# Optimization experiments

Measured on AMD Instinct MI355X. Metric: run time of the kernel, lower is better.

The kernel has to match this reference:

```python
import jax, jax.numpy as jnp
import numpy as np

N_NODES = 100000
NEG_SLOPE = 0.01  # F.leaky_relu default


def _hetero_graphconv(x, src, dst, W, b, n_nodes):
    """HeteroGraphConv(aggregate='sum') of DGL GraphConv(norm='both') per edge type.

    x: [N, d_in]; src/dst: [R, E] int; W: [R, d_in, d_out]; b: [R, d_out].
    """
    n_rel = W.shape[0]
    ones = None
    out = jnp.zeros((n_nodes, W.shape[2]), dtype=x.dtype)
    for r in range(n_rel):  # small fixed number of relations
        s, d = src[r], dst[r]
        e_ones = jnp.ones(s.shape, dtype=x.dtype)
        deg_out = jnp.clip(jax.ops.segment_sum(e_ones, s, num_segments=n_nodes), 1.0)
        deg_in = jnp.clip(jax.ops.segment_sum(e_ones, d, num_segments=n_nodes), 1.0)
        # norm='both': scale src by out_deg^-1/2, aggregate, scale dst by in_deg^-1/2.
        # Apply weight before gather (aggregation is linear) to shrink edge traffic.
        h = (x * (deg_out ** -0.5)[:, None]) @ W[r]          # [N, d_out]
        agg = jax.ops.segment_sum(h[s], d, num_segments=n_nodes)  # gather-scatter over edges
        out = out + agg * (deg_in ** -0.5)[:, None] + b[r]
    return out


def setup_inputs() -> dict:
    key = jax.random.key(0)
    ks = jax.random.split(key, 8)
    d_in, d_h, d_out, n_cls, n_rel, n_edges = 256, 128, 128, 16, 3, 600000
    x = jax.random.normal(ks[0], (N_NODES, d_in), dtype=jnp.float32)
    src = jax.random.randint(ks[1], (n_rel, n_edges), 0, N_NODES, dtype=jnp.int32)
    dst = jax.random.randint(ks[2], (n_rel, n_edges), 0, N_NODES, dtype=jnp.int32)
    W0 = jax.random.normal(ks[3], (n_rel, d_in, d_h), dtype=jnp.float32) * (d_in ** -0.5)
    b0 = jnp.zeros((n_rel, d_h), dtype=jnp.float32)
    W1 = jax.random.normal(ks[4], (n_rel, d_h, d_out), dtype=jnp.float32) * (d_h ** -0.5)
    b1 = jnp.zeros((n_rel, d_out), dtype=jnp.float32)
    fc_W = jax.random.normal(ks[5], (d_out, n_cls), dtype=jnp.float32) * (d_out ** -0.5)
    fc_b = jnp.zeros((n_cls,), dtype=jnp.float32)
    return {"x": x, "src": src, "dst": dst, "W0": W0, "b0": b0,
            "W1": W1, "b1": b1, "fc_W": fc_W, "fc_b": fc_b}


def reference(x, src, dst, W0, b0, W1, b1, fc_W, fc_b):
    n = x.shape[0]
    h = _hetero_graphconv(x, src, dst, W0, b0, n)
    h = jax.nn.leaky_relu(h, negative_slope=NEG_SLOPE)  # dropout rate 0 (eval)
    h = _hetero_graphconv(h, src, dst, W1, b1, n)       # last layer: no activation
    logits = h @ fc_W + fc_b
    return (h, logits)
```

## Files before the change

kernel.cpp:

```cpp
#include <hip/hip_runtime.h>
#include <hip/hip_bf16.h>
#include <stdint.h>


typedef __attribute__((ext_vector_type(8))) short bf16x8;
typedef __attribute__((ext_vector_type(4))) float f32x4;
typedef unsigned short u16;

#define SCAN_T 256
#define SCAN_E 8
#define SCAN_BLK (SCAN_T * SCAN_E)
#define CUR_PAD 16
#define BF_K 8
#define HIST_K 4
#define NSLOT 12

__global__ __launch_bounds__(256)
void hist_kernel(const int* __restrict__ src, const int* __restrict__ dst,
                 int* __restrict__ cnt_out8, int* __restrict__ cnt_in8,
                 int E, int N) {
    int r = blockIdx.y;
    int e0 = blockIdx.x * (256 * HIST_K) + threadIdx.x;
    int copy = blockIdx.x & 7;
    size_t base = ((size_t)copy * 3 + r) * N;
    int s[HIST_K], d[HIST_K];
#pragma unroll
    for (int j = 0; j < HIST_K; j++) {
        int e = e0 + j * 256;
        bool v = e < E;
        s[j] = v ? src[(size_t)r * E + e] : -1;
        d[j] = v ? dst[(size_t)r * E + e] : -1;
    }
#pragma unroll
    for (int j = 0; j < HIST_K; j++)
        if (s[j] >= 0) atomicAdd(cnt_out8 + base + s[j], 1);
#pragma unroll
    for (int j = 0; j < HIST_K; j++)
        if (d[j] >= 0) atomicAdd(cnt_in8 + base + d[j], 1);
}

__global__ __launch_bounds__(256)
void reduce_scales_kernel(const int* __restrict__ cnt_out8, const int* __restrict__ cnt_in8,
                          float* __restrict__ s_out, float* __restrict__ s_in,
                          int* __restrict__ cnt_all, int N) {
    int n = blockIdx.x * blockDim.x + threadIdx.x;
    if (n >= N) return;
    int tot = 0;
#pragma unroll
    for (int r = 0; r < 3; r++) {
        int co = 0, ci = 0;
#pragma unroll
        for (int c = 0; c < 8; c++) {
            co += cnt_out8[((size_t)c * 3 + r) * N + n];
            ci += cnt_in8[((size_t)c * 3 + r) * N + n];
        }
        s_out[(size_t)r * N + n] = rsqrtf(fmaxf((float)co, 1.0f));
        s_in[(size_t)r * N + n]  = rsqrtf(fmaxf((float)ci, 1.0f));
        tot += ci;
    }
    cnt_all[n] = tot;
}

__global__ __launch_bounds__(SCAN_T)
void scan1_kernel(const int* __restrict__ cnt, int* __restrict__ pre,
                  int* __restrict__ bsums, int N) {
    int b = blockIdx.x, t = threadIdx.x;
    int base = b * SCAN_BLK + t * SCAN_E;
    int v[SCAN_E], s = 0;
#pragma unroll
    for (int j = 0; j < SCAN_E; j++) {
        int idx = base + j;
        v[j] = (idx < N) ? cnt[idx] : 0;
        s += v[j];
    }
    __shared__ int sd[SCAN_T];
    sd[t] = s;
    __syncthreads();
    for (int off = 1; off < SCAN_T; off <<= 1) {
        int x = (t >= off) ? sd[t - off] : 0;
        __syncthreads();
        sd[t] += x;
        __syncthreads();
    }
    if (t == SCAN_T - 1) bsums[b] = sd[t];
    int run = sd[t] - s;
#pragma unroll
    for (int j = 0; j < SCAN_E; j++) {
        int idx = base + j;
        if (idx < N) pre[idx] = run;
        run += v[j];
    }
}

__global__ void scan2_kernel(int* __restrict__ bsums, int* __restrict__ row_start,
                             int nb, int N) {
    int run = 0;
    for (int b = 0; b < nb; b++) {
        int t = bsums[b];
        bsums[b] = run;
        run += t;
    }
    row_start[N] = run;
}

__global__ __launch_bounds__(SCAN_T)
void scan3_kernel(int* __restrict__ pre, const int* __restrict__ bsums,
                  int* __restrict__ cursor, int nb, int N) {
    int b = blockIdx.x, t = threadIdx.x;
    int add = bsums[b];
    int base = b * SCAN_BLK + t * SCAN_E;
#pragma unroll
    for (int j = 0; j < SCAN_E; j++) {
        int idx = base + j;
        if (idx < N) {
            int val = pre[idx] + add;
            pre[idx] = val;
            cursor[(size_t)idx * CUR_PAD] = val;
        }
    }
}

__global__ __launch_bounds__(256)
void bucket_fill_kernel(const int* __restrict__ src, const int* __restrict__ dst,
                        int* __restrict__ cursor, int* __restrict__ esrc,
                        int E, int N) {
    int r = blockIdx.y;
    int e0 = blockIdx.x * (256 * BF_K) + threadIdx.x;
    int s[BF_K], d[BF_K], pos[BF_K];
#pragma unroll
    for (int j = 0; j < BF_K; j++) {
        int e = e0 + j * 256;
        bool v = e < E;
        s[j] = v ? src[(size_t)r * E + e] : -1;
        d[j] = v ? dst[(size_t)r * E + e] : 0;
    }
#pragma unroll
    for (int j = 0; j < BF_K; j++)
        pos[j] = (s[j] >= 0) ? atomicAdd(cursor + (size_t)d[j] * CUR_PAD, 1) : 0;
#pragma unroll
    for (int j = 0; j < BF_K; j++)
        if (s[j] >= 0) esrc[pos[j]] = r * N + s[j];
}

__global__ __launch_bounds__(256)
void prep_w_kernel(const float* __restrict__ W0, const float* __restrict__ W1,
                   u16* __restrict__ w0hi, u16* __restrict__ w0lo,
                   u16* __restrict__ w1hi, u16* __restrict__ w1lo) {
    int idx = blockIdx.x * blockDim.x + threadIdx.x;
    const int n0 = 3 * 256 * 128;
    const int n1 = 3 * 128 * 128;
    if (idx >= n0 + n1) return;
    float f;
    u16 *phi, *plo;
    int oidx;
    if (idx < n0) {
        int r = idx / 32768, rem = idx % 32768;
        int n = rem / 256, k = rem % 256;
        f = W0[(size_t)r * 32768 + (size_t)k * 128 + n];
        phi = w0hi; plo = w0lo; oidx = idx;
    } else {
        int i2 = idx - n0;
        int r = i2 / 16384, rem = i2 % 16384;
        int n = rem / 128, k = rem % 128;
        f = W1[(size_t)r * 16384 + (size_t)k * 128 + n];
        phi = w1hi; plo = w1lo; oidx = i2;
    }
    uint32_t u = __float_as_uint(f);
    phi[oidx] = (u16)(u >> 16);
    float lo = f - __uint_as_float(u & 0xFFFF0000u);
    uint32_t ul = __float_as_uint(lo);
    plo[oidx] = (u16)((ul + 0x7FFFu + ((ul >> 16) & 1u)) >> 16);
}

__global__ __launch_bounds__(256)
void gemm_split_bf16(const float* __restrict__ A, const float* __restrict__ s_out,
                     const u16* __restrict__ Whi_all, const u16* __restrict__ Wlo_all,
                     u16* __restrict__ Cout_all, int M, int K, int Nn) {
    const int r = blockIdx.y;
    const float* scale = s_out + (size_t)r * Nn;
    const u16* Whi = Whi_all + (size_t)r * K * 128;
    const u16* Wlo = Wlo_all + (size_t)r * K * 128;
    u16* Cout = Cout_all + (size_t)r * Nn * 128;

    __shared__ u16 As_hi[128][40];
    __shared__ u16 As_lo[128][40];
    __shared__ u16 Bs_hi[128][40];
    __shared__ u16 Bs_lo[128][40];

    const int tid  = threadIdx.x;
    const int m0   = blockIdx.x * 128;
    const int lane = tid & 63;
    const int wave = tid >> 6;
    const int wm   = (wave & 1) * 64;
    const int wn   = (wave >> 1) * 64;
    const int lm   = lane & 15;
    const int kq   = (lane >> 4) * 8;

    f32x4 acc[4][4];
#pragma unroll
    for (int i = 0; i < 4; i++)
#pragma unroll
        for (int j = 0; j < 4; j++) acc[i][j] = (f32x4){0.f, 0.f, 0.f, 0.f};

    const int srow = tid >> 1;
    const int skb  = (tid & 1) * 16;

    const bool valid = (m0 + srow) < M;
    const float sval = valid ? scale[m0 + srow] : 0.f;
    const float* arow = A + (size_t)(m0 + srow) * K;
    const u16* whrow = Whi + (size_t)srow * K;
    const u16* wlrow = Wlo + (size_t)srow * K;

    for (int k0 = 0; k0 < K; k0 += 32) {
        float fa[16];
        if (valid) {
            *(float4*)&fa[0]  = *(const float4*)(arow + k0 + skb);
            *(float4*)&fa[4]  = *(const float4*)(arow + k0 + skb + 4);
            *(float4*)&fa[8]  = *(const float4*)(arow + k0 + skb + 8);
            *(float4*)&fa[12] = *(const float4*)(arow + k0 + skb + 12);
        } else {
#pragma unroll
            for (int i = 0; i < 16; i++) fa[i] = 0.f;
        }
        uint32_t ah[8], al[8];
#pragma unroll
        for (int p = 0; p < 8; p++) {
            float f0 = fa[2 * p] * sval, f1 = fa[2 * p + 1] * sval;
            uint32_t u0 = __float_as_uint(f0), u1 = __float_as_uint(f1);
            ah[p] = (u0 >> 16) | (u1 & 0xFFFF0000u);
            float l0 = f0 - __uint_as_float(u0 & 0xFFFF0000u);
            float l1 = f1 - __uint_as_float(u1 & 0xFFFF0000u);
            al[p] = (__float_as_uint(l0) >> 16) | (__float_as_uint(l1) & 0xFFFF0000u);
        }
        *(uint4*)&As_hi[srow][skb]     = *(uint4*)&ah[0];
        *(uint4*)&As_hi[srow][skb + 8] = *(uint4*)&ah[4];
        *(uint4*)&As_lo[srow][skb]     = *(uint4*)&al[0];
        *(uint4*)&As_lo[srow][skb + 8] = *(uint4*)&al[4];

        *(uint4*)&Bs_hi[srow][skb]     = *(const uint4*)(whrow + k0 + skb);
        *(uint4*)&Bs_hi[srow][skb + 8] = *(const uint4*)(whrow + k0 + skb + 8);
        *(uint4*)&Bs_lo[srow][skb]     = *(const uint4*)(wlrow + k0 + skb);
        *(uint4*)&Bs_lo[srow][skb + 8] = *(const uint4*)(wlrow + k0 + skb + 8);

        __syncthreads();

        bf16x8 a_hi[4], a_lo[4], b_hi[4], b_lo[4];
#pragma unroll
        for (int i = 0; i < 4; i++) {
            a_hi[i] = *(const bf16x8*)&As_hi[wm + i * 16 + lm][kq];
            a_lo[i] = *(const bf16x8*)&As_lo[wm + i * 16 + lm][kq];
            b_hi[i] = *(const bf16x8*)&Bs_hi[wn + i * 16 + lm][kq];
            b_lo[i] = *(const bf16x8*)&Bs_lo[wn + i * 16 + lm][kq];
        }
#pragma unroll
        for (int i = 0; i < 4; i++)
#pragma unroll
            for (int j = 0; j < 4; j++) {
                acc[i][j] = __builtin_amdgcn_mfma_f32_16x16x32_bf16(a_hi[i], b_hi[j], acc[i][j], 0, 0, 0);
                acc[i][j] = __builtin_amdgcn_mfma_f32_16x16x32_bf16(a_lo[i], b_hi[j], acc[i][j], 0, 0, 0);
                acc[i][j] = __builtin_amdgcn_mfma_f32_16x16x32_bf16(a_hi[i], b_lo[j], acc[i][j], 0, 0, 0);
            }
        __syncthreads();
    }

    const int rq = (lane >> 4) * 4;
#pragma unroll
    for (int i = 0; i < 4; i++) {
        int mbase = m0 + wm + i * 16 + rq;
#pragma unroll
        for (int j = 0; j < 4; j++) {
            int col = wn + j * 16 + lm;
#pragma unroll
            for (int rg = 0; rg < 4; rg++) {
                int m = mbase + rg;
                if (m < M) {
                    uint32_t u = __float_as_uint(acc[i][j][rg]);
                    Cout[(size_t)m * 128 + col] =
                        (u16)((u + 0x7FFFu + ((u >> 16) & 1u)) >> 16);
                }
            }
        }
    }
}

#define BF16_LO(u) __uint_as_float((u) << 16)
#define BF16_HI(u) __uint_as_float((u) & 0xFFFF0000u)

__device__ __forceinline__ void gather_pair(const uint32_t* __restrict__ hb32,
                                            const int* __restrict__ row_start,
                                            const int* __restrict__ esrc,
                                            const float* __restrict__ s_in,
                                            int snodeA, int nodeBr, int half,
                                            int lane31, int N, float acc[4]) {
    const int N2 = N * 2;
    const int snodeB = (nodeBr < N) ? nodeBr : (N - 1);
    const int begA = __builtin_amdgcn_readfirstlane(row_start[snodeA]);
    const int endA = __builtin_amdgcn_readfirstlane(row_start[snodeA + 1]);
    const int begB = __builtin_amdgcn_readfirstlane(row_start[snodeB]);
    const int endB = __builtin_amdgcn_readfirstlane(row_start[snodeB + 1]);
    const int degA = endA - begA, degB = endB - begB;
    const int maxdeg = degA > degB ? degA : degB;

    float wA0 = s_in[snodeA], wA1 = s_in[(size_t)N + snodeA], wA2 = s_in[(size_t)N2 + snodeA];
    float wB0 = s_in[snodeB], wB1 = s_in[(size_t)N + snodeB], wB2 = s_in[(size_t)N2 + snodeB];
    if (nodeBr >= N) { wB0 = 0.f; wB1 = 0.f; wB2 = 0.f; }

    const float w0 = half ? wB0 : wA0;
    const float w1 = half ? wB1 : wA1;
    const float w2 = half ? wB2 : wA2;
    const int   deg = half ? degB : degA;
    const uint32_t* hcol = hb32 + lane31 * 2;

    for (int j = 0; j < maxdeg; j += NSLOT) {
        uint2 u[NSLOT];
        float w[NSLOT];
#pragma unroll
        for (int p = 0; p < NSLOT; p++) {
            int iA = esrc[begA + j + p];
            int iB = esrc[begB + j + p];
            int idx = half ? iB : iA;
            float ws = (idx < N) ? w0 : ((idx < N2) ? w1 : w2);
            bool act = (j + p) < deg;
            w[p] = act ? ws : 0.f;
            idx = act ? idx : 0;
            u[p] = *(const uint2*)(hcol + (size_t)idx * 64);
        }
#pragma unroll
        for (int p = 0; p < NSLOT; p++) {
            acc[0] = fmaf(BF16_LO(u[p].x), w[p], acc[0]);
            acc[1] = fmaf(BF16_HI(u[p].x), w[p], acc[1]);
            acc[2] = fmaf(BF16_LO(u[p].y), w[p], acc[2]);
            acc[3] = fmaf(BF16_HI(u[p].y), w[p], acc[3]);
        }
    }
}

__global__ __launch_bounds__(256)
void gather_l0(const u16* __restrict__ hb, const int* __restrict__ row_start,
               const int* __restrict__ esrc, const float* __restrict__ s_in,
               const float* __restrict__ b, float* __restrict__ out, int N) {
    int wv = threadIdx.x >> 6;
    int t = threadIdx.x & 63;
    int half = t >> 5;
    int lane31 = t & 31;
    int snodeA = __builtin_amdgcn_readfirstlane(blockIdx.x * 8 + wv * 2);
    if (snodeA >= N) return;
    int nodeBr = snodeA + 1;
    float acc[4] = {0.f, 0.f, 0.f, 0.f};
    gather_pair((const uint32_t*)hb, row_start, esrc, s_in,
                snodeA, nodeBr, half, lane31, N, acc);
    int node = half ? nodeBr : snodeA;
    int c0 = lane31 * 4;
    float4 b0v = *(const float4*)(b + c0);
    float4 b1v = *(const float4*)(b + 128 + c0);
    float4 b2v = *(const float4*)(b + 256 + c0);
    float bs[4] = {b0v.x + b1v.x + b2v.x, b0v.y + b1v.y + b2v.y,
                   b0v.z + b1v.z + b2v.z, b0v.w + b1v.w + b2v.w};
    float4 o;
    float* po = (float*)&o;
#pragma unroll
    for (int k = 0; k < 4; k++) {
        float v = acc[k] + bs[k];
        po[k] = fmaxf(v, 0.f) + 0.01f * fminf(v, 0.f);
    }
    if (node < N) *(float4*)(out + (size_t)node * 128 + c0) = o;
}

__global__ __launch_bounds__(256)
void gather_l1(const u16* __restrict__ hb, const int* __restrict__ row_start,
               const int* __restrict__ esrc, const float* __restrict__ s_in,
               const float* __restrict__ b, const float* __restrict__ fcW,
               const float* __restrict__ fcb, float* __restrict__ out_h,
               float* __restrict__ out_logits, int N) {
    int wv = threadIdx.x >> 6;
    int t = threadIdx.x & 63;
    int half = t >> 5;
    int lane31 = t & 31;
    int snodeA = __builtin_amdgcn_readfirstlane(blockIdx.x * 8 + wv * 2);
    if (snodeA >= N) return;
    int nodeBr = snodeA + 1;
    float acc[4] = {0.f, 0.f, 0.f, 0.f};
    gather_pair((const uint32_t*)hb, row_start, esrc, s_in,
                snodeA, nodeBr, half, lane31, N, acc);
    int node = half ? nodeBr : snodeA;
    int c0 = lane31 * 4;
    float4 b0v = *(const float4*)(b + c0);
    float4 b1v = *(const float4*)(b + 128 + c0);
    float4 b2v = *(const float4*)(b + 256 + c0);
    float v[4] = {acc[0] + b0v.x + b1v.x + b2v.x, acc[1] + b0v.y + b1v.y + b2v.y,
                  acc[2] + b0v.z + b1v.z + b2v.z, acc[3] + b0v.w + b1v.w + b2v.w};
    if (node < N) {
        float4 o = make_float4(v[0], v[1], v[2], v[3]);
        *(float4*)(out_h + (size_t)node * 128 + c0) = o;
    }

    float p[16];
#pragma unroll
    for (int jj = 0; jj < 16; jj++) {
        p[jj] = v[0] * fcW[(size_t)(c0 + 0) * 16 + jj]
              + v[1] * fcW[(size_t)(c0 + 1) * 16 + jj]
              + v[2] * fcW[(size_t)(c0 + 2) * 16 + jj]
              + v[3] * fcW[(size_t)(c0 + 3) * 16 + jj];
    }
#pragma unroll
    for (int off = 1; off <= 16; off <<= 1) {
#pragma unroll
        for (int jj = 0; jj < 16; jj++) p[jj] += __shfl_xor(p[jj], off);
    }
    if (lane31 == 0 && node < N) {
        float* lp = out_logits + (size_t)node * 16;
        *(float4*)(lp + 0)  = make_float4(p[0] + fcb[0],  p[1] + fcb[1],  p[2] + fcb[2],  p[3] + fcb[3]);
        *(float4*)(lp + 4)  = make_float4(p[4] + fcb[4],  p[5] + fcb[5],  p[6] + fcb[6],  p[7] + fcb[7]);
        *(float4*)(lp + 8)  = make_float4(p[8] + fcb[8],  p[9] + fcb[9],  p[10] + fcb[10], p[11] + fcb[11]);
        *(float4*)(lp + 12) = make_float4(p[12] + fcb[12], p[13] + fcb[13], p[14] + fcb[14], p[15] + fcb[15]);
    }
}

extern "C" void kernel_launch(void* const* d_in, const int* in_sizes, int n_in,
                              void* d_out, int out_size, void* d_ws, size_t ws_size,
                              hipStream_t stream) {
    const float* x   = (const float*)d_in[0];
    const int*   src = (const int*)d_in[1];
    const int*   dst = (const int*)d_in[2];
    const float* W0  = (const float*)d_in[3];
    const float* b0  = (const float*)d_in[4];
    const float* W1  = (const float*)d_in[5];
    const float* b1  = (const float*)d_in[6];
    const float* fcW = (const float*)d_in[7];
    const float* fcb = (const float*)d_in[8];

    const int N = in_sizes[0] / 256;
    const int E = in_sizes[1] / 3;
    const int nb = (N + SCAN_BLK - 1) / SCAN_BLK;

    float* out_h      = (float*)d_out;
    float* out_logits = out_h + (size_t)N * 128;

    char* p = (char*)d_ws;
    auto alloc = [&](size_t bytes) -> char* {
        char* q = p;
        p += (bytes + 255) & ~(size_t)255;
        return q;
    };
    float* s_out     = (float*)alloc(3 * (size_t)N * 4);
    float* s_in      = (float*)alloc(3 * (size_t)N * 4);
    int*   cnt8      = (int*)alloc(2 * 8 * 3 * (size_t)N * 4);
    int*   cnt_out8  = cnt8;
    int*   cnt_in8   = cnt8 + 8 * 3 * (size_t)N;
    int*   cnt_all   = (int*)alloc((size_t)N * 4);
    int*   row_start = (int*)alloc((size_t)(N + 1) * 4);
    int*   cursor    = (int*)alloc((size_t)N * CUR_PAD * 4);
    int*   bsums     = (int*)alloc(1024 * 4);
    int*   esrc      = (int*)alloc(3 * (size_t)E * 4 + 1024);
    u16*   w0hi      = (u16*)alloc(3 * 256 * 128 * 2);
    u16*   w0lo      = (u16*)alloc(3 * 256 * 128 * 2);
    u16*   w1hi      = (u16*)alloc(3 * 128 * 128 * 2);
    u16*   w1lo      = (u16*)alloc(3 * 128 * 128 * 2);
    u16*   hb        = (u16*)alloc(3 * (size_t)N * 128 * 2);
    float* acc0      = (float*)alloc((size_t)N * 128 * 4);

    hipMemsetAsync(cnt8, 0, 2 * 8 * 3 * (size_t)N * sizeof(int), stream);

    hist_kernel<<<dim3((E + 256 * HIST_K - 1) / (256 * HIST_K), 3), 256, 0, stream>>>(
        src, dst, cnt_out8, cnt_in8, E, N);
    reduce_scales_kernel<<<(N + 255) / 256, 256, 0, stream>>>(
        cnt_out8, cnt_in8, s_out, s_in, cnt_all, N);

    scan1_kernel<<<nb, SCAN_T, 0, stream>>>(cnt_all, row_start, bsums, N);
    scan2_kernel<<<1, 1, 0, stream>>>(bsums, row_start, nb, N);
    scan3_kernel<<<nb, SCAN_T, 0, stream>>>(row_start, bsums, cursor, nb, N);
    bucket_fill_kernel<<<dim3((E + 256 * BF_K - 1) / (256 * BF_K), 3), 256, 0, stream>>>(
        src, dst, cursor, esrc, E, N);

    prep_w_kernel<<<(3 * 256 * 128 + 3 * 128 * 128 + 255) / 256, 256, 0, stream>>>(
        W0, W1, w0hi, w0lo, w1hi, w1lo);

    int gemm_blocks   = (N + 127) / 128;
    int gather_blocks = (N + 7) / 8;

    gemm_split_bf16<<<dim3(gemm_blocks, 3), 256, 0, stream>>>(
        x, s_out, w0hi, w0lo, hb, N, 256, N);
    gather_l0<<<gather_blocks, 256, 0, stream>>>(hb, row_start, esrc, s_in, b0, acc0, N);

    gemm_split_bf16<<<dim3(gemm_blocks, 3), 256, 0, stream>>>(
        acc0, s_out, w1hi, w1lo, hb, N, 128, N);
    gather_l1<<<gather_blocks, 256, 0, stream>>>(hb, row_start, esrc, s_in, b1, fcW, fcb,
                                                 out_h, out_logits, N);
}
```

Before: 768.1 us.

## Merge per-relation GEMMs into one block sharing A tile; move out-degree scale to gather

The three per-relation GEMM launches are merged into one 768-thread block. The A tile (x or acc0) is loaded and split into hi/lo bf16 once and shared by three wave groups, each using its own relation's weights, which cuts A reads and conversion work by three. Because the A tile is now shared, the per-relation out-degree scale can no longer be applied to it, so it moves into the gather as a per-edge multiply by s_out[src]. This adds an extra scattered load per edge. Output stores in the last layer become nontemporal.

```diff
diff --git a/kernel.cpp b/kernel.cpp
--- a/kernel.cpp
+++ b/kernel.cpp
@@ -172,27 +172,23 @@
     plo[oidx] = (u16)((ul + 0x7FFFu + ((ul >> 16) & 1u)) >> 16);
 }
 
-__global__ __launch_bounds__(256)
-void gemm_split_bf16(const float* __restrict__ A, const float* __restrict__ s_out,
-                     const u16* __restrict__ Whi_all, const u16* __restrict__ Wlo_all,
-                     u16* __restrict__ Cout_all, int M, int K, int Nn) {
-    const int r = blockIdx.y;
-    const float* scale = s_out + (size_t)r * Nn;
-    const u16* Whi = Whi_all + (size_t)r * K * 128;
-    const u16* Wlo = Wlo_all + (size_t)r * K * 128;
-    u16* Cout = Cout_all + (size_t)r * Nn * 128;
-
+__global__ __launch_bounds__(768)
+void gemm_merged(const float* __restrict__ A,
+                 const u16* __restrict__ Whi_all, const u16* __restrict__ Wlo_all,
+                 u16* __restrict__ Cout_all, int M, int K, int Nn) {
     __shared__ u16 As_hi[128][40];
     __shared__ u16 As_lo[128][40];
-    __shared__ u16 Bs_hi[128][40];
-    __shared__ u16 Bs_lo[128][40];
+    __shared__ u16 Bs_hi[3][128][40];
+    __shared__ u16 Bs_lo[3][128][40];
 
     const int tid  = threadIdx.x;
     const int m0   = blockIdx.x * 128;
     const int lane = tid & 63;
     const int wave = tid >> 6;
-    const int wm   = (wave & 1) * 64;
-    const int wn   = (wave >> 1) * 64;
+    const int wr   = wave >> 2;
+    const int wq   = wave & 3;
+    const int wm   = (wq & 1) * 64;
+    const int wn   = (wq >> 1) * 64;
     const int lm   = lane & 15;
     const int kq   = (lane >> 4) * 8;
 
@@ -202,46 +198,57 @@
 #pragma unroll
         for (int j = 0; j < 4; j++) acc[i][j] = (f32x4){0.f, 0.f, 0.f, 0.f};
 
-    const int srow = tid >> 1;
-    const int skb  = (tid & 1) * 16;
-
-    const bool valid = (m0 + srow) < M;
-    const float sval = valid ? scale[m0 + srow] : 0.f;
-    const float* arow = A + (size_t)(m0 + srow) * K;
-    const u16* whrow = Whi + (size_t)srow * K;
-    const u16* wlrow = Wlo + (size_t)srow * K;
+    const int srowA = tid >> 1;
+    const int skbA  = (tid & 1) * 16;
+    const bool validA = (tid < 256) && ((m0 + srowA) < M);
+    const float* arow = A + (size_t)(m0 + srowA) * K;
+
+    const int bslot = tid - 256;
 
     for (int k0 = 0; k0 < K; k0 += 32) {
-        float fa[16];
-        if (valid) {
-            *(float4*)&fa[0]  = *(const float4*)(arow + k0 + skb);
-            *(float4*)&fa[4]  = *(const float4*)(arow + k0 + skb + 4);
-            *(float4*)&fa[8]  = *(const float4*)(arow + k0 + skb + 8);
-            *(float4*)&fa[12] = *(const float4*)(arow + k0 + skb + 12);
+        if (tid < 256) {
+            float fa[16];
+            if (validA) {
+                *(float4*)&fa[0]  = *(const float4*)(arow + k0 + skbA);
+                *(float4*)&fa[4]  = *(const float4*)(arow + k0 + skbA + 4);
+                *(float4*)&fa[8]  = *(const float4*)(arow + k0 + skbA + 8);
+                *(float4*)&fa[12] = *(const float4*)(arow + k0 + skbA + 12);
+            } else {
+#pragma unroll
+                for (int i = 0; i < 16; i++) fa[i] = 0.f;
+            }
+            uint32_t ah[8], al[8];
+#pragma unroll
+            for (int p = 0; p < 8; p++) {
+                float f0 = fa[2 * p], f1 = fa[2 * p + 1];
+                uint32_t u0 = __float_as_uint(f0), u1 = __float_as_uint(f1);
+                ah[p] = (u0 >> 16) | (u1 & 0xFFFF0000u);
+                float l0 = f0 - __uint_as_float(u0 & 0xFFFF0000u);
+                float l1 = f1 - __uint_as_float(u1 & 0xFFFF0000u);
+                al[p] = (__float_as_uint(l0) >> 16) | (__float_as_uint(l1) & 0xFFFF0000u);
+            }
+            *(uint4*)&As_hi[srowA][skbA]     = *(uint4*)&ah[0];
+            *(uint4*)&As_hi[srowA][skbA + 8] = *(uint4*)&ah[4];
+            *(uint4*)&As_lo[srowA][skbA]     = *(uint4*)&al[0];
+            *(uint4*)&As_lo[srowA][skbA + 8] = *(uint4*)&al[4];
         } else {
 #pragma unroll
-            for (int i = 0; i < 16; i++) fa[i] = 0.f;
-        }
-        uint32_t ah[8], al[8];
-#pragma unroll
-        for (int p = 0; p < 8; p++) {
-            float f0 = fa[2 * p] * sval, f1 = fa[2 * p + 1] * sval;
-            uint32_t u0 = __float_as_uint(f0), u1 = __float_as_uint(f1);
-            ah[p] = (u0 >> 16) | (u1 & 0xFFFF0000u);
-            float l0 = f0 - __uint_as_float(u0 & 0xFFFF0000u);
-            float l1 = f1 - __uint_as_float(u1 & 0xFFFF0000u);
-            al[p] = (__float_as_uint(l0) >> 16) | (__float_as_uint(l1) & 0xFFFF0000u);
-        }
-        *(uint4*)&As_hi[srow][skb]     = *(uint4*)&ah[0];
-        *(uint4*)&As_hi[srow][skb + 8] = *(uint4*)&ah[4];
-        *(uint4*)&As_lo[srow][skb]     = *(uint4*)&al[0];
-        *(uint4*)&As_lo[srow][skb + 8] = *(uint4*)&al[4];
-
-        *(uint4*)&Bs_hi[srow][skb]     = *(const uint4*)(whrow + k0 + skb);
-        *(uint4*)&Bs_hi[srow][skb + 8] = *(const uint4*)(whrow + k0 + skb + 8);
-        *(uint4*)&Bs_lo[srow][skb]     = *(const uint4*)(wlrow + k0 + skb);
-        *(uint4*)&Bs_lo[srow][skb + 8] = *(const uint4*)(wlrow + k0 + skb + 8);
-
+            for (int c = 0; c < 2; c++) {
+                int slot = bslot + c * 512;
+                if (slot < 768) {
+                    int r    = slot >> 8;
+                    int s2   = slot & 255;
+                    int srow = s2 >> 1;
+                    int skb  = (s2 & 1) * 16;
+                    const u16* wh = Whi_all + ((size_t)r * 128 + srow) * K;
+                    const u16* wl = Wlo_all + ((size_t)r * 128 + srow) * K;
+                    *(uint4*)&Bs_hi[r][srow][skb]     = *(const uint4*)(wh + k0 + skb);
+                    *(uint4*)&Bs_hi[r][srow][skb + 8] = *(const uint4*)(wh + k0 + skb + 8);
+                    *(uint4*)&Bs_lo[r][srow][skb]     = *(const uint4*)(wl + k0 + skb);
+                    *(uint4*)&Bs_lo[r][srow][skb + 8] = *(const uint4*)(wl + k0 + skb + 8);
+                }
+            }
+        }
         __syncthreads();
 
         bf16x8 a_hi[4], a_lo[4], b_hi[4], b_lo[4];
@@ -249,8 +256,8 @@
         for (int i = 0; i < 4; i++) {
             a_hi[i] = *(const bf16x8*)&As_hi[wm + i * 16 + lm][kq];
             a_lo[i] = *(const bf16x8*)&As_lo[wm + i * 16 + lm][kq];
-            b_hi[i] = *(const bf16x8*)&Bs_hi[wn + i * 16 + lm][kq];
-            b_lo[i] = *(const bf16x8*)&Bs_lo[wn + i * 16 + lm][kq];
+            b_hi[i] = *(const bf16x8*)&Bs_hi[wr][wn + i * 16 + lm][kq];
+            b_lo[i] = *(const bf16x8*)&Bs_lo[wr][wn + i * 16 + lm][kq];
         }
 #pragma unroll
         for (int i = 0; i < 4; i++)
@@ -263,6 +270,7 @@
         __syncthreads();
     }
 
+    u16* Cout = Cout_all + (size_t)wr * Nn * 128;
     const int rq = (lane >> 4) * 4;
 #pragma unroll
     for (int i = 0; i < 4; i++) {
@@ -290,6 +298,7 @@
                                             const int* __restrict__ row_start,
                                             const int* __restrict__ esrc,
                                             const float* __restrict__ s_in,
+                                            const float* __restrict__ s_out,
                                             int snodeA, int nodeBr, int half,
                                             int lane31, int N, float acc[4]) {
     const int N2 = N * 2;
@@ -321,8 +330,9 @@
             int idx = half ? iB : iA;
             float ws = (idx < N) ? w0 : ((idx < N2) ? w1 : w2);
             bool act = (j + p) < deg;
-            w[p] = act ? ws : 0.f;
             idx = act ? idx : 0;
+            float so = s_out[idx];
+            w[p] = act ? ws * so : 0.f;
             u[p] = *(const uint2*)(hcol + (size_t)idx * 64);
         }
 #pragma unroll
@@ -338,6 +348,7 @@
 __global__ __launch_bounds__(256)
 void gather_l0(const u16* __restrict__ hb, const int* __restrict__ row_start,
                const int* __restrict__ esrc, const float* __restrict__ s_in,
+               const float* __restrict__ s_out,
                const float* __restrict__ b, float* __restrict__ out, int N) {
     int wv = threadIdx.x >> 6;
     int t = threadIdx.x & 63;
@@ -347,7 +358,7 @@
     if (snodeA >= N) return;
     int nodeBr = snodeA + 1;
     float acc[4] = {0.f, 0.f, 0.f, 0.f};
-    gather_pair((const uint32_t*)hb, row_start, esrc, s_in,
+    gather_pair((const uint32_t*)hb, row_start, esrc, s_in, s_out,
                 snodeA, nodeBr, half, lane31, N, acc);
     int node = half ? nodeBr : snodeA;
     int c0 = lane31 * 4;
@@ -356,19 +367,19 @@
     float4 b2v = *(const float4*)(b + 256 + c0);
     float bs[4] = {b0v.x + b1v.x + b2v.x, b0v.y + b1v.y + b2v.y,
                    b0v.z + b1v.z + b2v.z, b0v.w + b1v.w + b2v.w};
-    float4 o;
-    float* po = (float*)&o;
+    f32x4 o;
 #pragma unroll
     for (int k = 0; k < 4; k++) {
         float v = acc[k] + bs[k];
-        po[k] = fmaxf(v, 0.f) + 0.01f * fminf(v, 0.f);
-    }
-    if (node < N) *(float4*)(out + (size_t)node * 128 + c0) = o;
+        o[k] = fmaxf(v, 0.f) + 0.01f * fminf(v, 0.f);
+    }
+    if (node < N) *(f32x4*)(out + (size_t)node * 128 + c0) = o;
 }
 
 __global__ __launch_bounds__(256)
 void gather_l1(const u16* __restrict__ hb, const int* __restrict__ row_start,
                const int* __restrict__ esrc, const float* __restrict__ s_in,
+               const float* __restrict__ s_out,
                const float* __restrict__ b, const float* __restrict__ fcW,
                const float* __restrict__ fcb, float* __restrict__ out_h,
                float* __restrict__ out_logits, int N) {
@@ -380,7 +391,7 @@
     if (snodeA >= N) return;
     int nodeBr = snodeA + 1;
     float acc[4] = {0.f, 0.f, 0.f, 0.f};
-    gather_pair((const uint32_t*)hb, row_start, esrc, s_in,
+    gather_pair((const uint32_t*)hb, row_start, esrc, s_in, s_out,
                 snodeA, nodeBr, half, lane31, N, acc);
     int node = half ? nodeBr : snodeA;
     int c0 = lane31 * 4;
@@ -390,8 +401,8 @@
     float v[4] = {acc[0] + b0v.x + b1v.x + b2v.x, acc[1] + b0v.y + b1v.y + b2v.y,
                   acc[2] + b0v.z + b1v.z + b2v.z, acc[3] + b0v.w + b1v.w + b2v.w};
     if (node < N) {
-        float4 o = make_float4(v[0], v[1], v[2], v[3]);
-        *(float4*)(out_h + (size_t)node * 128 + c0) = o;
+        f32x4 o = {v[0], v[1], v[2], v[3]};
+        __builtin_nontemporal_store(o, (f32x4*)(out_h + (size_t)node * 128 + c0));
     }
 
     float p[16];
@@ -409,10 +420,14 @@
     }
     if (lane31 == 0 && node < N) {
         float* lp = out_logits + (size_t)node * 16;
-        *(float4*)(lp + 0)  = make_float4(p[0] + fcb[0],  p[1] + fcb[1],  p[2] + fcb[2],  p[3] + fcb[3]);
-        *(float4*)(lp + 4)  = make_float4(p[4] + fcb[4],  p[5] + fcb[5],  p[6] + fcb[6],  p[7] + fcb[7]);
-        *(float4*)(lp + 8)  = make_float4(p[8] + fcb[8],  p[9] + fcb[9],  p[10] + fcb[10], p[11] + fcb[11]);
-        *(float4*)(lp + 12) = make_float4(p[12] + fcb[12], p[13] + fcb[13], p[14] + fcb[14], p[15] + fcb[15]);
+        f32x4 q0 = {p[0] + fcb[0],  p[1] + fcb[1],  p[2] + fcb[2],  p[3] + fcb[3]};
+        f32x4 q1 = {p[4] + fcb[4],  p[5] + fcb[5],  p[6] + fcb[6],  p[7] + fcb[7]};
+        f32x4 q2 = {p[8] + fcb[8],  p[9] + fcb[9],  p[10] + fcb[10], p[11] + fcb[11]};
+        f32x4 q3 = {p[12] + fcb[12], p[13] + fcb[13], p[14] + fcb[14], p[15] + fcb[15]};
+        __builtin_nontemporal_store(q0, (f32x4*)(lp + 0));
+        __builtin_nontemporal_store(q1, (f32x4*)(lp + 4));
+        __builtin_nontemporal_store(q2, (f32x4*)(lp + 8));
+        __builtin_nontemporal_store(q3, (f32x4*)(lp + 12));
     }
 }
 
@@ -478,12 +493,11 @@
     int gemm_blocks   = (N + 127) / 128;
     int gather_blocks = (N + 7) / 8;
 
-    gemm_split_bf16<<<dim3(gemm_blocks, 3), 256, 0, stream>>>(
-        x, s_out, w0hi, w0lo, hb, N, 256, N);
-    gather_l0<<<gather_blocks, 256, 0, stream>>>(hb, row_start, esrc, s_in, b0, acc0, N);
-
-    gemm_split_bf16<<<dim3(gemm_blocks, 3), 256, 0, stream>>>(
-        acc0, s_out, w1hi, w1lo, hb, N, 128, N);
-    gather_l1<<<gather_blocks, 256, 0, stream>>>(hb, row_start, esrc, s_in, b1, fcW, fcb,
-                                                 out_h, out_logits, N);
-}
+    gemm_merged<<<gemm_blocks, 768, 0, stream>>>(x, w0hi, w0lo, hb, N, 256, N);
+    gather_l0<<<gather_blocks, 256, 0, stream>>>(hb, row_start, esrc, s_in, s_out,
+                                                 b0, acc0, N);
+
+    gemm_merged<<<gemm_blocks, 768, 0, stream>>>(acc0, w1hi, w1lo, hb, N, 128, N);
+    gather_l1<<<gather_blocks, 256, 0, stream>>>(hb, row_start, esrc, s_in, s_out,
+                                                 b1, fcW, fcb, out_h, out_logits, N);
+}
```

Result: slower. 801.4 us (+4.3%).
